# Kernel tuning notes

Hardware: AMD Instinct MI355X
Metric: run time of the kernel (lower is better)

Reference implementation:

```python
import jax, jax.numpy as jnp
import numpy as np

N, H, O, E = 32768, 512, 512, 16


def setup_inputs() -> dict:
    key = jax.random.key(0)
    k0, k1, k2 = jax.random.split(key, 3)
    x = jax.random.normal(k0, (N, H), dtype=jnp.float32)
    # gate Linear(H -> E)
    Wg = jax.random.normal(k1, (E, H), dtype=jnp.float32) * (1.0 / np.sqrt(H))
    bg = jnp.zeros((E,), dtype=jnp.float32)
    # expert Linears(H -> O), stacked [E, O, H]
    We = jax.random.normal(k2, (E, O, H), dtype=jnp.float32) * (1.0 / np.sqrt(H))
    be = jnp.zeros((E, O), dtype=jnp.float32)
    return {"x": x, "Wg": Wg, "bg": bg, "We": We, "be": be}


def reference(x, Wg, bg, We, be):
    # gate: softmax over experts, then top-1 (argmax)
    logits = x @ Wg.T + bg                       # [N, E]
    weights = jax.nn.softmax(logits, axis=-1)
    expert_idx = jnp.argmax(weights, axis=-1)    # [N]
    # run every expert on every token, then select the top-1 expert's output.
    # (note: original module does NOT scale output by the gate weight)
    all_out = jnp.einsum('nh,eoh->neo', x, We) + be[None]   # [N, E, O]
    out = jnp.take_along_axis(all_out, expert_idx[:, None, None], axis=1)[:, 0]  # [N, O]
    return out
```

## Files before the change

### kernel.cpp

```cpp
#include <hip/hip_runtime.h>
#include <hip/hip_bf16.h>
#include <stdint.h>

#define NTOK 32768
#define HDIM 512
#define ODIM 512
#define NEXP 16

#define TM 128
#define TN 128
#define BK 64
#define MTILES 32

#define CSTRIDE 32

typedef __bf16 bf16x8 __attribute__((ext_vector_type(8)));
typedef float  floatx4 __attribute__((ext_vector_type(4)));

__device__ __forceinline__ unsigned pk2(unsigned lo, unsigned hi) {
  return (lo >> 16) | (hi & 0xffff0000u);
}

__device__ __forceinline__ bf16x8 asbf8(uint4 u) { bf16x8 v; __builtin_memcpy(&v, &u, 16); return v; }

__device__ __forceinline__ void split3(float4 a, float4 b, uint4* H, uint4* M, uint4* L) {
  float f[8] = {a.x, a.y, a.z, a.w, b.x, b.y, b.z, b.w};
  unsigned h[8], m[8], l[8];
#pragma unroll
  for (int j = 0; j < 8; ++j) {
    union { float F; unsigned U; } u; u.F = f[j];
    h[j] = u.U & 0xffff0000u;
    union { unsigned U; float F; } hv; hv.U = h[j];
    float r1 = f[j] - hv.F;
    union { float F; unsigned U; } r1u; r1u.F = r1;
    m[j] = r1u.U & 0xffff0000u;
    union { unsigned U; float F; } mv; mv.U = m[j];
    float r2 = r1 - mv.F;
    union { float F; unsigned U; } r2u; r2u.F = r2;
    l[j] = r2u.U;
  }
  H->x = pk2(h[0], h[1]); H->y = pk2(h[2], h[3]); H->z = pk2(h[4], h[5]); H->w = pk2(h[6], h[7]);
  M->x = pk2(m[0], m[1]); M->y = pk2(m[2], m[3]); M->z = pk2(m[4], m[5]); M->w = pk2(m[6], m[7]);
  L->x = pk2(l[0], l[1]); L->y = pk2(l[2], l[3]); L->z = pk2(l[4], l[5]); L->w = pk2(l[6], l[7]);
}

#define GLDS16(g, l) __builtin_amdgcn_global_load_lds( \
    (const __attribute__((address_space(1))) unsigned int*)(g), \
    (__attribute__((address_space(3))) unsigned int*)(l), 16, 0, 0)

__global__ __launch_bounds__(256) void cvt_we_kernel(const float* __restrict__ We,
                                                     unsigned short* __restrict__ out) {
  int i = blockIdx.x * 256 + threadIdx.x;
  const float4* src = (const float4*)We;
  float4 a = src[2 * i];
  float4 b = src[2 * i + 1];
  union { float F; unsigned U; } t[8] = {{a.x},{a.y},{a.z},{a.w},{b.x},{b.y},{b.z},{b.w}};
  uint4 o;
  o.x = pk2(t[0].U, t[1].U); o.y = pk2(t[2].U, t[3].U);
  o.z = pk2(t[4].U, t[5].U); o.w = pk2(t[6].U, t[7].U);
  ((uint4*)out)[i] = o;
}

__global__ __launch_bounds__(256, 2) void gate_kernel(const float* __restrict__ x,
                                                      const float* __restrict__ Wg,
                                                      const float* __restrict__ bg,
                                                      int* __restrict__ counts,
                                                      int* __restrict__ buckets,
                                                      unsigned short* __restrict__ xbf) {
  __shared__ __align__(16) unsigned short whf[16][64][8];
  __shared__ __align__(16) unsigned short wmf[16][64][8];
  __shared__ __align__(16) unsigned short wlf[16][64][8];
  __shared__ __align__(16) float red[4][4][16][20];

  int t = threadIdx.x;
  int lane = t & 63;
  int w = t >> 6;
  int tok0 = blockIdx.x * 64;

#pragma unroll
  for (int q = 0; q < 4; ++q) {
    int id = q * 256 + t;
    int s = id >> 6;
    int l = id & 63;
    const float* src = Wg + (size_t)(l & 15) * HDIM + s * 32 + (l >> 4) * 8;
    float4 a = *(const float4*)src;
    float4 b = *(const float4*)(src + 4);
    uint4 H, M, L;
    split3(a, b, &H, &M, &L);
    *(uint4*)&whf[s][l][0] = H;
    *(uint4*)&wmf[s][l][0] = M;
    *(uint4*)&wlf[s][l][0] = L;
  }
  __syncthreads();

  int fr = lane & 15;
  int quad = lane >> 4;
  floatx4 acc[4] = {};

  const float* xbase[4];
#pragma unroll
  for (int mt = 0; mt < 4; ++mt)
    xbase[mt] = x + (size_t)(tok0 + mt * 16 + fr) * HDIM + (w * 4) * 32 + quad * 8;

  float4 xa[4], xb[4];
#pragma unroll
  for (int mt = 0; mt < 4; ++mt) {
    xa[mt] = *(const float4*)(xbase[mt]);
    xb[mt] = *(const float4*)(xbase[mt] + 4);
  }

#pragma unroll
  for (int si = 0; si < 4; ++si) {
    int s = w * 4 + si;
    bf16x8 bh = *(const bf16x8*)&whf[s][lane][0];
    bf16x8 bm = *(const bf16x8*)&wmf[s][lane][0];
    bf16x8 bl = *(const bf16x8*)&wlf[s][lane][0];
    float4 na[4], nb[4];
    if (si < 3) {
#pragma unroll
      for (int mt = 0; mt < 4; ++mt) {
        na[mt] = *(const float4*)(xbase[mt] + (si + 1) * 32);
        nb[mt] = *(const float4*)(xbase[mt] + (si + 1) * 32 + 4);
      }
    }
#pragma unroll
    for (int mt = 0; mt < 4; ++mt) {
      size_t row = tok0 + mt * 16 + fr;
      uint4 H, M, L;
      split3(xa[mt], xb[mt], &H, &M, &L);
      *(uint4*)(xbf + row * HDIM + s * 32 + quad * 8) = H;
      bf16x8 ah = asbf8(H), am = asbf8(M), al = asbf8(L);
      acc[mt] = __builtin_amdgcn_mfma_f32_16x16x32_bf16(ah, bh, acc[mt], 0, 0, 0);
      acc[mt] = __builtin_amdgcn_mfma_f32_16x16x32_bf16(ah, bm, acc[mt], 0, 0, 0);
      acc[mt] = __builtin_amdgcn_mfma_f32_16x16x32_bf16(am, bh, acc[mt], 0, 0, 0);
      acc[mt] = __builtin_amdgcn_mfma_f32_16x16x32_bf16(am, bm, acc[mt], 0, 0, 0);
      acc[mt] = __builtin_amdgcn_mfma_f32_16x16x32_bf16(ah, bl, acc[mt], 0, 0, 0);
      acc[mt] = __builtin_amdgcn_mfma_f32_16x16x32_bf16(al, bh, acc[mt], 0, 0, 0);
      acc[mt] = __builtin_amdgcn_mfma_f32_16x16x32_bf16(am, bl, acc[mt], 0, 0, 0);
      acc[mt] = __builtin_amdgcn_mfma_f32_16x16x32_bf16(al, bm, acc[mt], 0, 0, 0);
    }
    if (si < 3) {
#pragma unroll
      for (int mt = 0; mt < 4; ++mt) { xa[mt] = na[mt]; xb[mt] = nb[mt]; }
    }
  }

#pragma unroll
  for (int mt = 0; mt < 4; ++mt)
#pragma unroll
    for (int i = 0; i < 4; ++i)
      red[w][mt][quad * 4 + i][fr] = acc[mt][i];
  __syncthreads();

  if (t < 64) {
    int tk = t;
    int mt = tk >> 4;
    int r = tk & 15;
    float4 tot4[4];
#pragma unroll
    for (int eq = 0; eq < 4; ++eq) tot4[eq] = *(const float4*)&bg[eq * 4];
#pragma unroll
    for (int ww = 0; ww < 4; ++ww)
#pragma unroll
      for (int eq = 0; eq < 4; ++eq) {
        float4 v = *(const float4*)&red[ww][mt][r][eq * 4];
        tot4[eq].x += v.x; tot4[eq].y += v.y; tot4[eq].z += v.z; tot4[eq].w += v.w;
      }
    float tot[16];
#pragma unroll
    for (int eq = 0; eq < 4; ++eq) {
      tot[eq * 4 + 0] = tot4[eq].x; tot[eq * 4 + 1] = tot4[eq].y;
      tot[eq * 4 + 2] = tot4[eq].z; tot[eq * 4 + 3] = tot4[eq].w;
    }
    float bv = tot[0]; int bi = 0;
#pragma unroll
    for (int e = 1; e < NEXP; ++e) if (tot[e] > bv) { bv = tot[e]; bi = e; }

    int token = tok0 + tk;
    for (int ee = 0; ee < NEXP; ++ee) {
      int e = (ee + blockIdx.x) & 15;
      unsigned long long mask = __ballot(bi == e);
      if (mask) {
        int leader = __builtin_ctzll(mask);
        int base = 0;
        if (lane == leader) base = atomicAdd(&counts[e << 5], (int)__popcll(mask));
        base = __shfl(base, leader, 64);
        if (bi == e) {
          int rank = (int)__popcll(mask & ((1ull << lane) - 1ull));
          buckets[e * NTOK + base + rank] = token;
        }
      }
    }
  }
}

__global__ __launch_bounds__(256, 2) void moe_gemm(const unsigned short* __restrict__ xbf,
                                                   const unsigned short* __restrict__ webf,
                                                   const float* __restrict__ be,
                                                   const int* __restrict__ counts,
                                                   const int* __restrict__ buckets,
                                                   float* __restrict__ out) {
  int e = blockIdx.z;
  int cnt = counts[e << 5];
  int m0 = blockIdx.x * TM;
  if (m0 >= cnt) return;
  int o0 = blockIdx.y * TN;

  __shared__ __align__(16) unsigned short As[2][TM * BK];
  __shared__ __align__(16) unsigned short Bs[2][TN * BK];
  __shared__ int toks[TM];

  int t = threadIdx.x;
  int lane = t & 63;
  int w = t >> 6;

  if (t < TM) {
    int r = m0 + t;
    toks[t] = (r < cnt) ? buckets[e * NTOK + r] : buckets[e * NTOK];
  }
  __syncthreads();

  int lrow = lane >> 3;
  int sig = lane & 7;
  int c = sig ^ lrow;
  const unsigned short* agp[4];
  const unsigned short* bgp[4];
#pragma unroll
  for (int i = 0; i < 4; ++i) {
    int row = w * 32 + i * 8 + lrow;
    agp[i] = xbf + (size_t)toks[row] * HDIM + c * 8;
    bgp[i] = webf + ((size_t)e * ODIM + o0 + row) * HDIM + c * 8;
  }

  int wm = (w & 1) * 64;
  int wn = (w >> 1) * 64;
  int fr = lane & 15;
  int quad = lane >> 4;
  int mconst[4], m7[4], nconst[4], n7[4];
#pragma unroll
  for (int mt = 0; mt < 4; ++mt) {
    int m = wm + mt * 16 + fr;
    mconst[mt] = (m >> 3) * 512 + (m & 7) * 64;
    m7[mt] = m & 7;
    int n = wn + mt * 16 + fr;
    nconst[mt] = (n >> 3) * 512 + (n & 7) * 64;
    n7[mt] = n & 7;
  }

  float bias[4];
#pragma unroll
  for (int nt = 0; nt < 4; ++nt)
    bias[nt] = be[e * ODIM + o0 + wn + nt * 16 + fr];

  floatx4 acc[4][4] = {};

#pragma unroll
  for (int i = 0; i < 4; ++i) {
    GLDS16(agp[i], As[0] + (w * 4 + i) * 512);
    GLDS16(bgp[i], Bs[0] + (w * 4 + i) * 512);
  }

  for (int k = 0; k < HDIM / BK; ++k) {
    int p = k & 1;
    __syncthreads();
    if (k < HDIM / BK - 1) {
      int koff = (k + 1) * BK;
#pragma unroll
      for (int i = 0; i < 4; ++i) {
        GLDS16(agp[i] + koff, As[1 - p] + (w * 4 + i) * 512);
        GLDS16(bgp[i] + koff, Bs[1 - p] + (w * 4 + i) * 512);
      }
    }

#pragma unroll
    for (int kk = 0; kk < 2; ++kk) {
      int cb = kk * 4 + quad;
      bf16x8 af[4], bf[4];
#pragma unroll
      for (int mt = 0; mt < 4; ++mt)
        af[mt] = *(const bf16x8*)(As[p] + mconst[mt] + ((cb ^ m7[mt]) << 3));
#pragma unroll
      for (int nt = 0; nt < 4; ++nt)
        bf[nt] = *(const bf16x8*)(Bs[p] + nconst[nt] + ((cb ^ n7[nt]) << 3));
#pragma unroll
      for (int mt = 0; mt < 4; ++mt)
#pragma unroll
        for (int nt = 0; nt < 4; ++nt)
          acc[mt][nt] = __builtin_amdgcn_mfma_f32_16x16x32_bf16(af[mt], bf[nt], acc[mt][nt], 0, 0, 0);
    }
  }

  int rbase = wm + quad * 4;
#pragma unroll
  for (int nt = 0; nt < 4; ++nt) {
    int col = o0 + wn + nt * 16 + fr;
#pragma unroll
    for (int mt = 0; mt < 4; ++mt) {
#pragma unroll
      for (int i = 0; i < 4; ++i) {
        int rl = rbase + mt * 16 + i;
        if (m0 + rl < cnt) {
          out[(size_t)toks[rl] * ODIM + col] = acc[mt][nt][i] + bias[nt];
        }
      }
    }
  }
}

#define WS_BUCKETS 4096
#define WS_XBF (WS_BUCKETS + NEXP * NTOK * 4)
#define WS_WEBF (WS_XBF + NTOK * HDIM * 2)

extern "C" void kernel_launch(void* const* d_in, const int* in_sizes, int n_in,
                              void* d_out, int out_size, void* d_ws, size_t ws_size,
                              hipStream_t stream) {
  const float* x  = (const float*)d_in[0];
  const float* Wg = (const float*)d_in[1];
  const float* bg = (const float*)d_in[2];
  const float* We = (const float*)d_in[3];
  const float* be = (const float*)d_in[4];
  float* out = (float*)d_out;
  char* ws = (char*)d_ws;

  int* counts = (int*)ws;
  int* buckets = (int*)(ws + WS_BUCKETS);
  unsigned short* xbf  = (unsigned short*)(ws + WS_XBF);
  unsigned short* webf = (unsigned short*)(ws + WS_WEBF);

  hipMemsetAsync(counts, 0, NEXP * CSTRIDE * 4, stream);
  cvt_we_kernel<<<NEXP * ODIM * HDIM / 8 / 256, 256, 0, stream>>>(We, webf);
  gate_kernel<<<NTOK / 64, 256, 0, stream>>>(x, Wg, bg, counts, buckets, xbf);
  moe_gemm<<<dim3(MTILES, ODIM / TN, NEXP), 256, 0, stream>>>(xbf, webf, be, counts, buckets, out);
}
```

Measured before the change: 210.5 us.

## Halve GEMM K-tile to 32 with new swizzled LDS layout and 4 blocks/CU

Reduces the K tile from 64 to 32, which halves the LDS footprint of the double-buffered A/B tiles, and raises launch bounds to request 4 blocks per CU. The LDS layout is reworked so that two rows are packed per 64-element line with an XOR swizzle, and the global-to-LDS load and fragment addressing are rewritten to match. The aim is higher occupancy for better latency hiding. The cost is twice as many K iterations and barriers, fewer MFMAs per sync, and tighter register limits that may cause spills.

```diff
diff --git a/kernel.cpp b/kernel.cpp
--- a/kernel.cpp
+++ b/kernel.cpp
@@ -9,7 +9,7 @@
 
 #define TM 128
 #define TN 128
-#define BK 64
+#define BK 32
 #define MTILES 32
 
 #define CSTRIDE 32
@@ -194,7 +194,7 @@
   }
 }
 
-__global__ __launch_bounds__(256, 2) void moe_gemm(const unsigned short* __restrict__ xbf,
+__global__ __launch_bounds__(256, 4) void moe_gemm(const unsigned short* __restrict__ xbf,
                                                    const unsigned short* __restrict__ webf,
                                                    const float* __restrict__ be,
                                                    const int* __restrict__ counts,
@@ -220,31 +220,34 @@
   }
   __syncthreads();
 
-  int lrow = lane >> 3;
-  int sig = lane & 7;
-  int c = sig ^ lrow;
-  const unsigned short* agp[4];
-  const unsigned short* bgp[4];
-#pragma unroll
-  for (int i = 0; i < 4; ++i) {
-    int row = w * 32 + i * 8 + lrow;
-    agp[i] = xbf + (size_t)toks[row] * HDIM + c * 8;
-    bgp[i] = webf + ((size_t)e * ODIM + o0 + row) * HDIM + c * 8;
+  int pl = lane >> 3;
+  int sl = lane & 7;
+  int slog = sl ^ pl;
+  int rsub = 2 * pl + (slog >> 2);
+  int cch = slog & 3;
+  const unsigned short* agp[2];
+  const unsigned short* bgp[2];
+#pragma unroll
+  for (int j = 0; j < 2; ++j) {
+    int row = w * 32 + j * 16 + rsub;
+    agp[j] = xbf + (size_t)toks[row] * HDIM + cch * 8;
+    bgp[j] = webf + ((size_t)e * ODIM + o0 + row) * HDIM + cch * 8;
   }
 
   int wm = (w & 1) * 64;
   int wn = (w >> 1) * 64;
   int fr = lane & 15;
   int quad = lane >> 4;
-  int mconst[4], m7[4], nconst[4], n7[4];
+
+  int aoff[4], boff[4];
 #pragma unroll
   for (int mt = 0; mt < 4; ++mt) {
     int m = wm + mt * 16 + fr;
-    mconst[mt] = (m >> 3) * 512 + (m & 7) * 64;
-    m7[mt] = m & 7;
+    int pr = m >> 1;
+    aoff[mt] = pr * 64 + (((((m & 1) << 2) | quad) ^ (pr & 7)) << 3);
     int n = wn + mt * 16 + fr;
-    nconst[mt] = (n >> 3) * 512 + (n & 7) * 64;
-    n7[mt] = n & 7;
+    int pn = n >> 1;
+    boff[mt] = pn * 64 + (((((n & 1) << 2) | quad) ^ (pn & 7)) << 3);
   }
 
   float bias[4];
@@ -254,10 +257,12 @@
 
   floatx4 acc[4][4] = {};
 
-#pragma unroll
-  for (int i = 0; i < 4; ++i) {
-    GLDS16(agp[i], As[0] + (w * 4 + i) * 512);
-    GLDS16(bgp[i], Bs[0] + (w * 4 + i) * 512);
+  int dst = w * 1024;
+
+#pragma unroll
+  for (int j = 0; j < 2; ++j) {
+    GLDS16(agp[j], As[0] + dst + j * 512);
+    GLDS16(bgp[j], Bs[0] + dst + j * 512);
   }
 
   for (int k = 0; k < HDIM / BK; ++k) {
@@ -266,28 +271,24 @@
     if (k < HDIM / BK - 1) {
       int koff = (k + 1) * BK;
 #pragma unroll
-      for (int i = 0; i < 4; ++i) {
-        GLDS16(agp[i] + koff, As[1 - p] + (w * 4 + i) * 512);
-        GLDS16(bgp[i] + koff, Bs[1 - p] + (w * 4 + i) * 512);
-      }
-    }
-
-#pragma unroll
-    for (int kk = 0; kk < 2; ++kk) {
-      int cb = kk * 4 + quad;
-      bf16x8 af[4], bf[4];
-#pragma unroll
-      for (int mt = 0; mt < 4; ++mt)
-        af[mt] = *(const bf16x8*)(As[p] + mconst[mt] + ((cb ^ m7[mt]) << 3));
+      for (int j = 0; j < 2; ++j) {
+        GLDS16(agp[j] + koff, As[1 - p] + dst + j * 512);
+        GLDS16(bgp[j] + koff, Bs[1 - p] + dst + j * 512);
+      }
+    }
+
+    bf16x8 af[4], bfr[4];
+#pragma unroll
+    for (int mt = 0; mt < 4; ++mt)
+      af[mt] = *(const bf16x8*)(As[p] + aoff[mt]);
+#pragma unroll
+    for (int nt = 0; nt < 4; ++nt)
+      bfr[nt] = *(const bf16x8*)(Bs[p] + boff[nt]);
+#pragma unroll
+    for (int mt = 0; mt < 4; ++mt)
 #pragma unroll
       for (int nt = 0; nt < 4; ++nt)
-        bf[nt] = *(const bf16x8*)(Bs[p] + nconst[nt] + ((cb ^ n7[nt]) << 3));
-#pragma unroll
-      for (int mt = 0; mt < 4; ++mt)
-#pragma unroll
-        for (int nt = 0; nt < 4; ++nt)
-          acc[mt][nt] = __builtin_amdgcn_mfma_f32_16x16x32_bf16(af[mt], bf[nt], acc[mt][nt], 0, 0, 0);
-    }
+        acc[mt][nt] = __builtin_amdgcn_mfma_f32_16x16x32_bf16(af[mt], bfr[nt], acc[mt][nt], 0, 0, 0);
   }
 
   int rbase = wm + quad * 4;
```

New measurement: 202.6 us. 1.04x faster.
